# Performance work log

Hardware: AMD Instinct MI355X
Metric: run time of the kernel (lower is better)

## Reference

```python
import jax, jax.numpy as jnp
import numpy as np

B, T, D, H = 4, 1024, 512, 8
DH = D // H
MLP = 4 * D
EPS = 1e-6


def _clinear(xr, xi, Wr, Wi, br, bi):
    # Naive complex Linear = two real nn.Linear layers (each adds its own bias):
    # re = Lr(xr) - Li(xi), im = Lr(xi) + Li(xr)
    re = xr @ Wr.T - xi @ Wi.T + (br - bi)
    im = xi @ Wr.T + xr @ Wi.T + (br + bi)
    return re, im


def _cln(xr, xi):
    # NaiveComplexLayerNorm: real LayerNorm (no affine) on re and im separately
    def ln(v):
        m = jnp.mean(v, -1, keepdims=True)
        va = jnp.var(v, -1, keepdims=True)
        return (v - m) * jax.lax.rsqrt(va + EPS)
    return ln(xr), ln(xi)


def _modulate(xr, xi, shr, shi, scr, sci):
    # complex x * (1 + scale) + shift, scale/shift are [B,D] broadcast over seq
    a, b = (1.0 + scr)[:, None, :], sci[:, None, :]
    return xr * a - xi * b + shr[:, None, :], xr * b + xi * a + shi[:, None, :]


def _gate(gr, gi, xr, xi):
    a, b = gr[:, None, :], gi[:, None, :]
    return xr * a - xi * b, xr * b + xi * a


def _heads(x):  # [B,T,D] -> [B,H,T,DH]
    return x.reshape(B, T, H, DH).transpose(0, 2, 1, 3)


def reference(x_re, x_im, c_re, c_im,
              ada_Wr, ada_Wi, ada_br, ada_bi,
              q_Wr, q_Wi, q_br, q_bi,
              k_Wr, k_Wi, k_br, k_bi,
              v_Wr, v_Wi, v_br, v_bi,
              o_Wr, o_Wi, o_br, o_bi,
              f1_Wr, f1_Wi, f1_br, f1_bi,
              f2_Wr, f2_Wi, f2_br, f2_bi):
    # adaLN_modulation: complex SiLU -> complex Linear -> 6 chunks along dim 1
    sr, si = jax.nn.silu(c_re), jax.nn.silu(c_im)
    mr, mi = _clinear(sr, si, ada_Wr, ada_Wi, ada_br, ada_bi)
    sh_ar, sc_ar, g_ar, sh_mr, sc_mr, g_mr = jnp.split(mr, 6, axis=1)
    sh_ai, sc_ai, g_ai, sh_mi, sc_mi, g_mi = jnp.split(mi, 6, axis=1)

    nr, ni = _cln(x_re, x_im)
    hr, hi = _modulate(nr, ni, sh_ar, sh_ai, sc_ar, sc_ai)

    qr, qi = _clinear(hr, hi, q_Wr, q_Wi, q_br, q_bi)
    kr, ki = _clinear(hr, hi, k_Wr, k_Wi, k_br, k_bi)
    vr, vi = _clinear(hr, hi, v_Wr, v_Wi, v_br, v_bi)
    qr, qi, kr, ki, vr, vi = map(_heads, (qr, qi, kr, ki, vr, vi))

    scale = 1.0 / jnp.sqrt(jnp.float32(DH))
    # complex scores q @ k^T (no conjugation, matching plain complex matmul)
    s_re = (jnp.einsum('bhqd,bhkd->bhqk', qr, kr) - jnp.einsum('bhqd,bhkd->bhqk', qi, ki)) * scale
    s_im = (jnp.einsum('bhqd,bhkd->bhqk', qr, ki) + jnp.einsum('bhqd,bhkd->bhqk', qi, kr)) * scale
    # naive complex softmax: real softmax applied to re/im independently
    a_re = jax.nn.softmax(s_re, axis=-1)
    a_im = jax.nn.softmax(s_im, axis=-1)
    o_r = jnp.einsum('bhqk,bhkd->bhqd', a_re, vr) - jnp.einsum('bhqk,bhkd->bhqd', a_im, vi)
    o_i = jnp.einsum('bhqk,bhkd->bhqd', a_re, vi) + jnp.einsum('bhqk,bhkd->bhqd', a_im, vr)
    o_r = o_r.transpose(0, 2, 1, 3).reshape(B, T, D)
    o_i = o_i.transpose(0, 2, 1, 3).reshape(B, T, D)
    o_r, o_i = _clinear(o_r, o_i, o_Wr, o_Wi, o_br, o_bi)

    gr, gi = _gate(g_ar, g_ai, o_r, o_i)
    x_re, x_im = x_re + gr, x_im + gi

    # ---- MLP branch
    nr, ni = _cln(x_re, x_im)
    hr, hi = _modulate(nr, ni, sh_mr, sh_mi, sc_mr, sc_mi)
    hr, hi = _clinear(hr, hi, f1_Wr, f1_Wi, f1_br, f1_bi)
    hr = jax.nn.gelu(hr, approximate=True)  # ComplexGELU(tanh) per component
    hi = jax.nn.gelu(hi, approximate=True)
    hr, hi = _clinear(hr, hi, f2_Wr, f2_Wi, f2_br, f2_bi)
    gr, gi = _gate(g_mr, g_mi, hr, hi)
    return jnp.stack([x_re + gr, x_im + gi])  # [2,B,T,D] = (real, imag)


def setup_inputs() -> dict:
    key = jax.random.key(0)
    ks = iter(jax.random.split(key, 48))

    def rn(shape, s=1.0):
        return jax.random.normal(next(ks), shape, dtype=jnp.float32) * s

    inp = {'x_re': rn((B, T, D)), 'x_im': rn((B, T, D)),
           'c_re': rn((B, D)), 'c_im': rn((B, D))}

    def lin(name, din, dout):
        inp[name + '_Wr'] = rn((dout, din), 0.02)
        inp[name + '_Wi'] = rn((dout, din), 0.02)
        inp[name + '_br'] = rn((dout,), 0.02)
        inp[name + '_bi'] = rn((dout,), 0.02)

    lin('ada', D, 6 * D)
    for n in ('q', 'k', 'v', 'o'):
        lin(n, D, D)
    lin('f1', D, MLP)
    lin('f2', MLP, D)
    return inp
```

## Files before the change

kernel.cpp:

```cpp
#include <hip/hip_runtime.h>


typedef unsigned short u16;
typedef __attribute__((ext_vector_type(8))) __bf16 bf16x8;
typedef __attribute__((ext_vector_type(8))) u16    u16x8;
typedef __attribute__((ext_vector_type(4))) u16    u16x4;
typedef __attribute__((ext_vector_type(4))) float  f32x4;

#define MFMA16(a, b, c) __builtin_amdgcn_mfma_f32_16x16x32_bf16(a, b, c, 0, 0, 0)

static constexpr int Bd = 4, Td = 1024, Dd = 512, Hd = 8, DHd = 64, MLPd = 2048;

__device__ __forceinline__ u16 f2bf(float x) {
  unsigned int u = __builtin_bit_cast(unsigned int, x);
  u += 0x7fffu + ((u >> 16) & 1u);
  return (u16)(u >> 16);
}
__device__ __forceinline__ bf16x8 ldsfrag(const u16* p) {
  return __builtin_bit_cast(bf16x8, *(const u16x8*)p);
}
__device__ __forceinline__ bf16x8 negbf(bf16x8 v) {
  u16x8 u = __builtin_bit_cast(u16x8, v);
  u ^= (u16)0x8000;
  return __builtin_bit_cast(bf16x8, u);
}
__device__ __forceinline__ float gelu_tanh(float x) {
  float t = tanhf(0.7978845608028654f * (x + 0.044715f * x * x * x));
  return 0.5f * x * (1.f + t);
}

struct CJobs {
  const float* src[12];
  u16* dst[12];
  int blk_start[13];
};
__global__ __launch_bounds__(256) void convert_kernel(CJobs J) {
  const int blk = blockIdx.x;
  int jj = 0;
  while (jj < 11 && blk >= J.blk_start[jj + 1]) ++jj;
  const int idx = (blk - J.blk_start[jj]) * 256 + threadIdx.x;
  const float4 v = ((const float4*)J.src[jj])[idx];
  u16x4 o;
  o[0] = f2bf(v.x); o[1] = f2bf(v.y); o[2] = f2bf(v.z); o[3] = f2bf(v.w);
  *(u16x4*)(J.dst[jj] + (size_t)idx * 4) = o;
}

__global__ __launch_bounds__(256) void ada_kernel(
    const float* __restrict__ c_re, const float* __restrict__ c_im,
    const float* __restrict__ Wr, const float* __restrict__ Wi,
    const float* __restrict__ br, const float* __restrict__ bi,
    float* __restrict__ m_r, float* __restrict__ m_i) {
  __shared__ __align__(16) float sr[512], si[512];
  const int b = blockIdx.x / 12, nb = blockIdx.x % 12;
  const int tid = threadIdx.x;
  for (int i = tid; i < 512; i += 256) {
    const float xr = c_re[b * 512 + i], xi = c_im[b * 512 + i];
    sr[i] = xr / (1.f + __expf(-xr));
    si[i] = xi / (1.f + __expf(-xi));
  }
  __syncthreads();
  const int n = nb * 256 + tid;
  const float4* wr4 = (const float4*)(Wr + (size_t)n * 512);
  const float4* wi4 = (const float4*)(Wi + (size_t)n * 512);
  const float4* sr4 = (const float4*)sr;
  const float4* si4 = (const float4*)si;
  float ar = 0.f, ai = 0.f;
  for (int k = 0; k < 128; ++k) {
    const float4 a_ = sr4[k], b_ = si4[k], u = wr4[k], v = wi4[k];
    ar += a_.x * u.x - b_.x * v.x + a_.y * u.y - b_.y * v.y +
          a_.z * u.z - b_.z * v.z + a_.w * u.w - b_.w * v.w;
    ai += b_.x * u.x + a_.x * v.x + b_.y * u.y + a_.y * v.y +
          b_.z * u.z + a_.z * v.z + b_.w * u.w + a_.w * v.w;
  }
  m_r[(size_t)b * 3072 + n] = ar + br[n] - bi[n];
  m_i[(size_t)b * 3072 + n] = ai + br[n] + bi[n];
}

__global__ __launch_bounds__(256) void ln_mod_kernel(
    const float* __restrict__ xr, const float* __restrict__ xi,
    const float* __restrict__ mv_r, const float* __restrict__ mv_i,
    int off_sh, int off_sc,
    u16* __restrict__ hr, u16* __restrict__ hi) {
  const int row = blockIdx.x;
  const int b = row >> 10;
  const int tid = threadIdx.x;
  const float* xrp = xr + (size_t)row * 512;
  const float* xip = xi + (size_t)row * 512;
  const float r0 = xrp[tid], r1 = xrp[tid + 256];
  const float i0 = xip[tid], i1 = xip[tid + 256];
  float s0 = r0 + r1, s1 = r0 * r0 + r1 * r1;
  float s2 = i0 + i1, s3 = i0 * i0 + i1 * i1;
  #pragma unroll
  for (int o = 32; o > 0; o >>= 1) {
    s0 += __shfl_down(s0, o); s1 += __shfl_down(s1, o);
    s2 += __shfl_down(s2, o); s3 += __shfl_down(s3, o);
  }
  __shared__ float red[4][4];
  if ((tid & 63) == 0) {
    const int wv = tid >> 6;
    red[wv][0] = s0; red[wv][1] = s1; red[wv][2] = s2; red[wv][3] = s3;
  }
  __syncthreads();
  s0 = red[0][0] + red[1][0] + red[2][0] + red[3][0];
  s1 = red[0][1] + red[1][1] + red[2][1] + red[3][1];
  s2 = red[0][2] + red[1][2] + red[2][2] + red[3][2];
  s3 = red[0][3] + red[1][3] + red[2][3] + red[3][3];
  const float mr = s0 * (1.f / 512.f), mi = s2 * (1.f / 512.f);
  const float vr = s1 * (1.f / 512.f) - mr * mr;
  const float vi = s3 * (1.f / 512.f) - mi * mi;
  const float rr = rsqrtf(vr + 1e-6f), ri = rsqrtf(vi + 1e-6f);
  const float* shr = mv_r + (size_t)b * 3072 + off_sh;
  const float* shi = mv_i + (size_t)b * 3072 + off_sh;
  const float* scr = mv_r + (size_t)b * 3072 + off_sc;
  const float* sci = mv_i + (size_t)b * 3072 + off_sc;
  #pragma unroll
  for (int jj = 0; jj < 2; ++jj) {
    const int n = tid + jj * 256;
    const float nr = ((jj ? r1 : r0) - mr) * rr;
    const float ni = ((jj ? i1 : i0) - mi) * ri;
    const float a = 1.f + scr[n], bb = sci[n];
    hr[(size_t)row * 512 + n] = f2bf(nr * a - ni * bb + shr[n]);
    hi[(size_t)row * 512 + n] = f2bf(nr * bb + ni * a + shi[n]);
  }
}

template <int EPI>
__global__ __launch_bounds__(256) void cgemm_kernel(
    const u16* __restrict__ Ar, const u16* __restrict__ Ai,
    const u16* __restrict__ W0r, const u16* __restrict__ W0i,
    const float* __restrict__ b0r, const float* __restrict__ b0i,
    const u16* __restrict__ W1r, const u16* __restrict__ W1i,
    const float* __restrict__ b1r, const float* __restrict__ b1i,
    const u16* __restrict__ W2r, const u16* __restrict__ W2i,
    const float* __restrict__ b2r, const float* __restrict__ b2i,
    int K, int ntiles_per_seg, int out_ld,
    u16* __restrict__ o0r, u16* __restrict__ o0i,
    u16* __restrict__ o1r, u16* __restrict__ o1i,
    u16* __restrict__ o2r, u16* __restrict__ o2i,
    const float* __restrict__ resid_r, const float* __restrict__ resid_i,
    const float* __restrict__ gate_r, const float* __restrict__ gate_i,
    float* __restrict__ ofr, float* __restrict__ ofi) {
  const int seg = blockIdx.y / ntiles_per_seg;
  const int n0 = (blockIdx.y % ntiles_per_seg) * 64;
  const int m0 = blockIdx.x * 64;
  const u16* Wr = (seg == 0) ? W0r : (seg == 1) ? W1r : W2r;
  const u16* Wi = (seg == 0) ? W0i : (seg == 1) ? W1i : W2i;
  const float* br = (seg == 0) ? b0r : (seg == 1) ? b1r : b2r;
  const float* bi = (seg == 0) ? b0i : (seg == 1) ? b1i : b2i;
  u16* obr = (seg == 0) ? o0r : (seg == 1) ? o1r : o2r;
  u16* obi = (seg == 0) ? o0i : (seg == 1) ? o1i : o2i;

  __shared__ __align__(16) u16 sA[2][64 * 72];
  __shared__ __align__(16) u16 sB[2][64 * 72];

  const int tid = threadIdx.x;
  const int w = tid >> 6, lane = tid & 63;
  const int wm = w >> 1, wn = w & 1;
  const int q4 = lane >> 4, c = lane & 15;

  const f32x4 z = {0.f, 0.f, 0.f, 0.f};
  f32x4 accR[2][2], accI[2][2];
  for (int a = 0; a < 2; ++a)
    for (int b2 = 0; b2 < 2; ++b2) { accR[a][b2] = z; accI[a][b2] = z; }

  for (int kt = 0; kt < K; kt += 64) {
    for (int idx = tid; idx < 512; idx += 256) {
      const int row = idx >> 3, cg = idx & 7;
      const int lo = row * 72 + cg * 8;
      *(u16x8*)&sA[0][lo] = *(const u16x8*)(Ar + (size_t)(m0 + row) * K + kt + cg * 8);
      *(u16x8*)&sA[1][lo] = *(const u16x8*)(Ai + (size_t)(m0 + row) * K + kt + cg * 8);
      *(u16x8*)&sB[0][lo] = *(const u16x8*)(Wr + (size_t)(n0 + row) * K + kt + cg * 8);
      *(u16x8*)&sB[1][lo] = *(const u16x8*)(Wi + (size_t)(n0 + row) * K + kt + cg * 8);
    }
    __syncthreads();
    #pragma unroll
    for (int kc = 0; kc < 2; ++kc) {
      bf16x8 a_r[2], a_i[2], a_n[2];
      #pragma unroll
      for (int mi = 0; mi < 2; ++mi) {
        const int off = (wm * 32 + mi * 16 + c) * 72 + kc * 32 + q4 * 8;
        a_r[mi] = ldsfrag(&sA[0][off]);
        a_i[mi] = ldsfrag(&sA[1][off]);
        a_n[mi] = negbf(a_i[mi]);
      }
      #pragma unroll
      for (int ni = 0; ni < 2; ++ni) {
        const int off = (wn * 32 + ni * 16 + c) * 72 + kc * 32 + q4 * 8;
        const bf16x8 b_r = ldsfrag(&sB[0][off]);
        const bf16x8 b_i = ldsfrag(&sB[1][off]);
        #pragma unroll
        for (int mi = 0; mi < 2; ++mi) {
          accR[mi][ni] = MFMA16(a_r[mi], b_r, accR[mi][ni]);
          accR[mi][ni] = MFMA16(a_n[mi], b_i, accR[mi][ni]);
          accI[mi][ni] = MFMA16(a_i[mi], b_r, accI[mi][ni]);
          accI[mi][ni] = MFMA16(a_r[mi], b_i, accI[mi][ni]);
        }
      }
    }
    __syncthreads();
  }

  const float scale = (EPI == 0 && seg == 0) ? 0.125f : 1.f;
  #pragma unroll
  for (int mi = 0; mi < 2; ++mi)
    #pragma unroll
    for (int ni = 0; ni < 2; ++ni) {
      const int n = n0 + wn * 32 + ni * 16 + c;
      const float biasr = br[n] - bi[n];
      const float biasi = br[n] + bi[n];
      #pragma unroll
      for (int r = 0; r < 4; ++r) {
        const int m = m0 + wm * 32 + mi * 16 + q4 * 4 + r;
        const float ore = accR[mi][ni][r] + biasr;
        const float oim = accI[mi][ni][r] + biasi;
        if (EPI == 0) {
          obr[(size_t)m * out_ld + n] = f2bf(ore * scale);
          obi[(size_t)m * out_ld + n] = f2bf(oim * scale);
        } else if (EPI == 2) {
          obr[(size_t)m * out_ld + n] = f2bf(gelu_tanh(ore));
          obi[(size_t)m * out_ld + n] = f2bf(gelu_tanh(oim));
        } else {
          const int bb = m >> 10;
          const float gr = gate_r[(size_t)bb * 3072 + n];
          const float gi = gate_i[(size_t)bb * 3072 + n];
          const size_t o = (size_t)m * 512 + n;
          ofr[o] = resid_r[o] + ore * gr - oim * gi;
          ofi[o] = resid_i[o] + ore * gi + oim * gr;
        }
      }
    }
}

__global__ __launch_bounds__(256) void attn_kernel(
    const u16* __restrict__ Qr, const u16* __restrict__ Qi,
    const u16* __restrict__ Kr, const u16* __restrict__ Ki,
    const u16* __restrict__ Vr, const u16* __restrict__ Vi,
    u16* __restrict__ Or, u16* __restrict__ Oi) {
  __shared__ __align__(16) u16 sQ[2][64 * 72];
  __shared__ __align__(16) u16 sK[2][64 * 72];
  __shared__ __align__(16) u16 sV[2][64 * 72];

  const int tid = threadIdx.x;
  const int w = tid >> 6, lane = tid & 63;
  const int q4 = lane >> 4, c = lane & 15;
  const int bh = blockIdx.y, b = bh >> 3, h = bh & 7;
  const int t0 = blockIdx.x * 64;
  const size_t base = (size_t)b * Td * Dd + h * DHd;

  for (int idx = tid; idx < 512; idx += 256) {
    const int row = idx >> 3, cg = idx & 7;
    const size_t g = base + (size_t)(t0 + row) * Dd + cg * 8;
    const int lo = row * 72 + cg * 8;
    *(u16x8*)&sQ[0][lo] = *(const u16x8*)(Qr + g);
    *(u16x8*)&sQ[1][lo] = *(const u16x8*)(Qi + g);
  }
  __syncthreads();
  bf16x8 aQr[2], aQi[2], aQn[2];
  #pragma unroll
  for (int kc = 0; kc < 2; ++kc) {
    const int off = (w * 16 + c) * 72 + kc * 32 + q4 * 8;
    aQr[kc] = ldsfrag(&sQ[0][off]);
    aQi[kc] = ldsfrag(&sQ[1][off]);
    aQn[kc] = negbf(aQi[kc]);
  }

  float mst[2][4], lst[2][4];
  #pragma unroll
  for (int p = 0; p < 2; ++p)
    for (int r = 0; r < 4; ++r) { mst[p][r] = -1e30f; lst[p][r] = 0.f; }
  const f32x4 z = {0.f, 0.f, 0.f, 0.f};
  f32x4 U1[4], U2[4], U3[4], U4[4];
  for (int i = 0; i < 4; ++i) { U1[i] = z; U2[i] = z; U3[i] = z; U4[i] = z; }

  for (int kt = 0; kt < 16; ++kt) {
    for (int idx = tid; idx < 512; idx += 256) {
      const int row = idx >> 3, cg = idx & 7;
      const size_t g = base + (size_t)(kt * 64 + row) * Dd + cg * 8;
      const int lo = row * 72 + cg * 8;
      *(u16x8*)&sK[0][lo] = *(const u16x8*)(Kr + g);
      *(u16x8*)&sK[1][lo] = *(const u16x8*)(Ki + g);
      const u16x8 vvr = *(const u16x8*)(Vr + g);
      const u16x8 vvi = *(const u16x8*)(Vi + g);
      #pragma unroll
      for (int j = 0; j < 8; ++j) {
        sV[0][(cg * 8 + j) * 72 + row] = vvr[j];
        sV[1][(cg * 8 + j) * 72 + row] = vvi[j];
      }
    }
    __syncthreads();

    f32x4 S[2][4];
    #pragma unroll
    for (int nb = 0; nb < 4; ++nb) {
      f32x4 tr = z, ti = z;
      #pragma unroll
      for (int kc = 0; kc < 2; ++kc) {
        const int off = (nb * 16 + c) * 72 + kc * 32 + q4 * 8;
        const bf16x8 bKr = ldsfrag(&sK[0][off]);
        const bf16x8 bKi = ldsfrag(&sK[1][off]);
        tr = MFMA16(aQr[kc], bKr, tr);
        tr = MFMA16(aQn[kc], bKi, tr);
        ti = MFMA16(aQi[kc], bKr, ti);
        ti = MFMA16(aQr[kc], bKi, ti);
      }
      S[0][nb] = tr; S[1][nb] = ti;
    }
    __syncthreads();

    float alpha[2][4];
    #pragma unroll
    for (int p = 0; p < 2; ++p) {
      float rs[4];
      #pragma unroll
      for (int r = 0; r < 4; ++r) {
        float tm = fmaxf(fmaxf(S[p][0][r], S[p][1][r]), fmaxf(S[p][2][r], S[p][3][r]));
        #pragma unroll
        for (int o = 1; o < 16; o <<= 1) tm = fmaxf(tm, __shfl_xor(tm, o));
        const float mn = fmaxf(mst[p][r], tm);
        alpha[p][r] = __expf(mst[p][r] - mn);
        mst[p][r] = mn;
        rs[r] = 0.f;
      }
      #pragma unroll
      for (int nb = 0; nb < 4; ++nb)
        #pragma unroll
        for (int r = 0; r < 4; ++r) {
          const float pv = __expf(S[p][nb][r] - mst[p][r]);
          rs[r] += pv;
          sK[p][(w * 16 + q4 * 4 + r) * 72 + nb * 16 + c] = f2bf(pv);
        }
      #pragma unroll
      for (int r = 0; r < 4; ++r) {
        float s = rs[r];
        #pragma unroll
        for (int o = 1; o < 16; o <<= 1) s += __shfl_xor(s, o);
        lst[p][r] = lst[p][r] * alpha[p][r] + s;
      }
    }
    #pragma unroll
    for (int i = 0; i < 4; ++i)
      #pragma unroll
      for (int r = 0; r < 4; ++r) {
        U1[i][r] *= alpha[0][r]; U2[i][r] *= alpha[0][r];
        U3[i][r] *= alpha[1][r]; U4[i][r] *= alpha[1][r];
      }
    asm volatile("s_waitcnt lgkmcnt(0)" ::: "memory");
    #pragma unroll
    for (int kc = 0; kc < 2; ++kc) {
      const int poff = (w * 16 + c) * 72 + kc * 32 + q4 * 8;
      const bf16x8 aPr = ldsfrag(&sK[0][poff]);
      const bf16x8 aPi = ldsfrag(&sK[1][poff]);
      #pragma unroll
      for (int nd = 0; nd < 4; ++nd) {
        const int voff = (nd * 16 + c) * 72 + kc * 32 + q4 * 8;
        const bf16x8 bVr = ldsfrag(&sV[0][voff]);
        const bf16x8 bVi = ldsfrag(&sV[1][voff]);
        U1[nd] = MFMA16(aPr, bVr, U1[nd]);
        U2[nd] = MFMA16(aPr, bVi, U2[nd]);
        U3[nd] = MFMA16(aPi, bVr, U3[nd]);
        U4[nd] = MFMA16(aPi, bVi, U4[nd]);
      }
    }
    __syncthreads();
  }

  #pragma unroll
  for (int nd = 0; nd < 4; ++nd)
    #pragma unroll
    for (int r = 0; r < 4; ++r) {
      const int trow = t0 + w * 16 + q4 * 4 + r;
      const int d = nd * 16 + c;
      const float ilre = 1.f / lst[0][r], ilim = 1.f / lst[1][r];
      const float ore = U1[nd][r] * ilre - U4[nd][r] * ilim;
      const float oim = U2[nd][r] * ilre + U3[nd][r] * ilim;
      const size_t g = base + (size_t)trow * Dd + d;
      Or[g] = f2bf(ore);
      Oi[g] = f2bf(oim);
    }
}

extern "C" void kernel_launch(void* const* d_in, const int* in_sizes, int n_in,
                              void* d_out, int out_size, void* d_ws, size_t ws_size,
                              hipStream_t stream) {
  const float* x_re  = (const float*)d_in[0];
  const float* x_im  = (const float*)d_in[1];
  const float* c_re  = (const float*)d_in[2];
  const float* c_im  = (const float*)d_in[3];
  const float* adaWr = (const float*)d_in[4];
  const float* adaWi = (const float*)d_in[5];
  const float* adabr = (const float*)d_in[6];
  const float* adabi = (const float*)d_in[7];
  const float* qWr = (const float*)d_in[8],  *qWi = (const float*)d_in[9];
  const float* qbr = (const float*)d_in[10], *qbi = (const float*)d_in[11];
  const float* kWr = (const float*)d_in[12], *kWi = (const float*)d_in[13];
  const float* kbr = (const float*)d_in[14], *kbi = (const float*)d_in[15];
  const float* vWr = (const float*)d_in[16], *vWi = (const float*)d_in[17];
  const float* vbr = (const float*)d_in[18], *vbi = (const float*)d_in[19];
  const float* oWr = (const float*)d_in[20], *oWi = (const float*)d_in[21];
  const float* obr = (const float*)d_in[22], *obi = (const float*)d_in[23];
  const float* f1Wr = (const float*)d_in[24], *f1Wi = (const float*)d_in[25];
  const float* f1br = (const float*)d_in[26], *f1bi = (const float*)d_in[27];
  const float* f2Wr = (const float*)d_in[28], *f2Wi = (const float*)d_in[29];
  const float* f2br = (const float*)d_in[30], *f2bi = (const float*)d_in[31];

  char* wsp = (char*)d_ws;
  size_t off = 0;
  auto alloc = [&](size_t bytes) -> void* {
    void* p = wsp + off;
    off += (bytes + 255) & ~(size_t)255;
    return p;
  };
  const size_t WQ = 512 * 512, WF = 2048 * 512;
  u16* wqr = (u16*)alloc(WQ * 2); u16* wqi = (u16*)alloc(WQ * 2);
  u16* wkr = (u16*)alloc(WQ * 2); u16* wki = (u16*)alloc(WQ * 2);
  u16* wvr = (u16*)alloc(WQ * 2); u16* wvi = (u16*)alloc(WQ * 2);
  u16* wor = (u16*)alloc(WQ * 2); u16* woi = (u16*)alloc(WQ * 2);
  u16* wf1r = (u16*)alloc(WF * 2); u16* wf1i = (u16*)alloc(WF * 2);
  u16* wf2r = (u16*)alloc(WF * 2); u16* wf2i = (u16*)alloc(WF * 2);
  float* m_r = (float*)alloc(4 * 3072 * 4);
  float* m_i = (float*)alloc(4 * 3072 * 4);
  const size_t ACT = (size_t)Bd * Td * Dd;
  u16* h1r = (u16*)alloc(ACT * 2); u16* h1i = (u16*)alloc(ACT * 2);
  u16* qbr_ = (u16*)alloc(ACT * 2); u16* qbi_ = (u16*)alloc(ACT * 2);
  u16* kbr_ = (u16*)alloc(ACT * 2); u16* kbi_ = (u16*)alloc(ACT * 2);
  u16* vbr_ = (u16*)alloc(ACT * 2); u16* vbi_ = (u16*)alloc(ACT * 2);
  u16* atr = (u16*)alloc(ACT * 2); u16* ati = (u16*)alloc(ACT * 2);
  float* x2r = (float*)alloc(ACT * 4); float* x2i = (float*)alloc(ACT * 4);
  u16* h2r = h1r; u16* h2i = h1i;
  u16* f1or = qbr_;
  u16* f1oi = qbr_ + (size_t)Bd * Td * MLPd;

  CJobs J;
  const float* wsrc[12] = {qWr, qWi, kWr, kWi, vWr, vWi, oWr, oWi, f1Wr, f1Wi, f2Wr, f2Wi};
  u16* wdst[12] = {wqr, wqi, wkr, wki, wvr, wvi, wor, woi, wf1r, wf1i, wf2r, wf2i};
  int cum = 0;
  for (int j = 0; j < 12; ++j) {
    J.src[j] = wsrc[j]; J.dst[j] = wdst[j]; J.blk_start[j] = cum;
    cum += (j < 8 ? (int)WQ : (int)WF) / 1024;
  }
  J.blk_start[12] = cum;
  convert_kernel<<<cum, 256, 0, stream>>>(J);

  ada_kernel<<<48, 256, 0, stream>>>(c_re, c_im, adaWr, adaWi, adabr, adabi, m_r, m_i);

  ln_mod_kernel<<<4096, 256, 0, stream>>>(x_re, x_im, m_r, m_i, 0, 512, h1r, h1i);

  cgemm_kernel<0><<<dim3(64, 24), 256, 0, stream>>>(
      h1r, h1i, wqr, wqi, qbr, qbi, wkr, wki, kbr, kbi, wvr, wvi, vbr, vbi,
      512, 8, 512, qbr_, qbi_, kbr_, kbi_, vbr_, vbi_,
      nullptr, nullptr, nullptr, nullptr, nullptr, nullptr);

  attn_kernel<<<dim3(16, 32), 256, 0, stream>>>(qbr_, qbi_, kbr_, kbi_, vbr_, vbi_, atr, ati);

  cgemm_kernel<1><<<dim3(64, 8), 256, 0, stream>>>(
      atr, ati, wor, woi, obr, obi, wor, woi, obr, obi, wor, woi, obr, obi,
      512, 8, 512, nullptr, nullptr, nullptr, nullptr, nullptr, nullptr,
      x_re, x_im, m_r + 1024, m_i + 1024, x2r, x2i);

  ln_mod_kernel<<<4096, 256, 0, stream>>>(x2r, x2i, m_r, m_i, 1536, 2048, h2r, h2i);

  cgemm_kernel<2><<<dim3(64, 32), 256, 0, stream>>>(
      h2r, h2i, wf1r, wf1i, f1br, f1bi, wf1r, wf1i, f1br, f1bi, wf1r, wf1i, f1br, f1bi,
      512, 32, 2048, f1or, f1oi, nullptr, nullptr, nullptr, nullptr,
      nullptr, nullptr, nullptr, nullptr, nullptr, nullptr);

  float* outp = (float*)d_out;
  cgemm_kernel<3><<<dim3(64, 8), 256, 0, stream>>>(
      f1or, f1oi, wf2r, wf2i, f2br, f2bi, wf2r, wf2i, f2br, f2bi, wf2r, wf2i, f2br, f2bi,
      2048, 8, 512, nullptr, nullptr, nullptr, nullptr, nullptr, nullptr,
      x2r, x2i, m_r + 2560, m_i + 2560, outp, outp + ACT);
}
```

Measured before the change: 459.4 us.

## Pre-transpose V in QKV epilogue and register-prefetch K/V tiles in attention

The V projection epilogue now writes V transposed per (batch, head) as [d][t] using vectorized stores, so the attention kernel can fill its V tile with plain 16-byte LDS writes instead of scalar transposing scatters. The attention kernel loads Q fragments straight from global memory into registers, dropping the sQ staging buffer and one barrier. It prefetches the next K/V tile into registers while the current tile is processed, restructures the barriers, and raises wave priority around the MFMA blocks. f2bf also switches to the compiler's native bf16 conversion. The launch code must pass the transposed V layout consistently.

```diff
diff --git a/kernel.cpp b/kernel.cpp
--- a/kernel.cpp
+++ b/kernel.cpp
@@ -12,9 +12,7 @@
 static constexpr int Bd = 4, Td = 1024, Dd = 512, Hd = 8, DHd = 64, MLPd = 2048;
 
 __device__ __forceinline__ u16 f2bf(float x) {
-  unsigned int u = __builtin_bit_cast(unsigned int, x);
-  u += 0x7fffu + ((u >> 16) & 1u);
-  return (u16)(u >> 16);
+  return __builtin_bit_cast(u16, (__bf16)x);
 }
 __device__ __forceinline__ bf16x8 ldsfrag(const u16* p) {
   return __builtin_bit_cast(bf16x8, *(const u16x8*)p);
@@ -208,6 +206,19 @@
       const int n = n0 + wn * 32 + ni * 16 + c;
       const float biasr = br[n] - bi[n];
       const float biasi = br[n] + bi[n];
+      if (EPI == 0 && seg == 2) {
+        const int m = m0 + wm * 32 + mi * 16 + q4 * 4;
+        u16x4 pr, pi;
+        #pragma unroll
+        for (int r = 0; r < 4; ++r) {
+          pr[r] = f2bf(accR[mi][ni][r] + biasr);
+          pi[r] = f2bf(accI[mi][ni][r] + biasi);
+        }
+        const size_t o = ((size_t)((m >> 10) * 512 + n)) * 1024 + (m & 1023);
+        *(u16x4*)(obr + o) = pr;
+        *(u16x4*)(obi + o) = pi;
+        continue;
+      }
       #pragma unroll
       for (int r = 0; r < 4; ++r) {
         const int m = m0 + wm * 32 + mi * 16 + q4 * 4 + r;
@@ -234,9 +245,8 @@
 __global__ __launch_bounds__(256) void attn_kernel(
     const u16* __restrict__ Qr, const u16* __restrict__ Qi,
     const u16* __restrict__ Kr, const u16* __restrict__ Ki,
-    const u16* __restrict__ Vr, const u16* __restrict__ Vi,
+    const u16* __restrict__ Vtr, const u16* __restrict__ Vti,
     u16* __restrict__ Or, u16* __restrict__ Oi) {
-  __shared__ __align__(16) u16 sQ[2][64 * 72];
   __shared__ __align__(16) u16 sK[2][64 * 72];
   __shared__ __align__(16) u16 sV[2][64 * 72];
 
@@ -246,21 +256,14 @@
   const int bh = blockIdx.y, b = bh >> 3, h = bh & 7;
   const int t0 = blockIdx.x * 64;
   const size_t base = (size_t)b * Td * Dd + h * DHd;
-
-  for (int idx = tid; idx < 512; idx += 256) {
-    const int row = idx >> 3, cg = idx & 7;
-    const size_t g = base + (size_t)(t0 + row) * Dd + cg * 8;
-    const int lo = row * 72 + cg * 8;
-    *(u16x8*)&sQ[0][lo] = *(const u16x8*)(Qr + g);
-    *(u16x8*)&sQ[1][lo] = *(const u16x8*)(Qi + g);
-  }
-  __syncthreads();
+  const size_t vbase = (size_t)bh << 16;
+
   bf16x8 aQr[2], aQi[2], aQn[2];
   #pragma unroll
   for (int kc = 0; kc < 2; ++kc) {
-    const int off = (w * 16 + c) * 72 + kc * 32 + q4 * 8;
-    aQr[kc] = ldsfrag(&sQ[0][off]);
-    aQi[kc] = ldsfrag(&sQ[1][off]);
+    const size_t g = base + (size_t)(t0 + w * 16 + c) * Dd + kc * 32 + q4 * 8;
+    aQr[kc] = __builtin_bit_cast(bf16x8, *(const u16x8*)(Qr + g));
+    aQi[kc] = __builtin_bit_cast(bf16x8, *(const u16x8*)(Qi + g));
     aQn[kc] = negbf(aQi[kc]);
   }
 
@@ -272,24 +275,45 @@
   f32x4 U1[4], U2[4], U3[4], U4[4];
   for (int i = 0; i < 4; ++i) { U1[i] = z; U2[i] = z; U3[i] = z; U4[i] = z; }
 
+  const int srow = tid >> 3, scg = tid & 7;
+  u16x8 R[2][4];
+  #pragma unroll
+  for (int it = 0; it < 2; ++it) {
+    const int row = srow + it * 32;
+    const size_t gk = base + (size_t)row * Dd + scg * 8;
+    const size_t gv = vbase + (size_t)row * Td + scg * 8;
+    R[it][0] = *(const u16x8*)(Kr + gk);
+    R[it][1] = *(const u16x8*)(Ki + gk);
+    R[it][2] = *(const u16x8*)(Vtr + gv);
+    R[it][3] = *(const u16x8*)(Vti + gv);
+  }
+
   for (int kt = 0; kt < 16; ++kt) {
-    for (int idx = tid; idx < 512; idx += 256) {
-      const int row = idx >> 3, cg = idx & 7;
-      const size_t g = base + (size_t)(kt * 64 + row) * Dd + cg * 8;
-      const int lo = row * 72 + cg * 8;
-      *(u16x8*)&sK[0][lo] = *(const u16x8*)(Kr + g);
-      *(u16x8*)&sK[1][lo] = *(const u16x8*)(Ki + g);
-      const u16x8 vvr = *(const u16x8*)(Vr + g);
-      const u16x8 vvi = *(const u16x8*)(Vi + g);
-      #pragma unroll
-      for (int j = 0; j < 8; ++j) {
-        sV[0][(cg * 8 + j) * 72 + row] = vvr[j];
-        sV[1][(cg * 8 + j) * 72 + row] = vvi[j];
-      }
-    }
     __syncthreads();
+    #pragma unroll
+    for (int it = 0; it < 2; ++it) {
+      const int lo = (srow + it * 32) * 72 + scg * 8;
+      *(u16x8*)&sK[0][lo] = R[it][0];
+      *(u16x8*)&sK[1][lo] = R[it][1];
+      *(u16x8*)&sV[0][lo] = R[it][2];
+      *(u16x8*)&sV[1][lo] = R[it][3];
+    }
+    if (kt < 15) {
+      #pragma unroll
+      for (int it = 0; it < 2; ++it) {
+        const int row = srow + it * 32;
+        const size_t gk = base + (size_t)((kt + 1) * 64 + row) * Dd + scg * 8;
+        const size_t gv = vbase + (size_t)row * Td + (kt + 1) * 64 + scg * 8;
+        R[it][0] = *(const u16x8*)(Kr + gk);
+        R[it][1] = *(const u16x8*)(Ki + gk);
+        R[it][2] = *(const u16x8*)(Vtr + gv);
+        R[it][3] = *(const u16x8*)(Vti + gv);
+      }
+    }
+    __syncthreads();
 
     f32x4 S[2][4];
+    __builtin_amdgcn_s_setprio(1);
     #pragma unroll
     for (int nb = 0; nb < 4; ++nb) {
       f32x4 tr = z, ti = z;
@@ -305,6 +329,7 @@
       }
       S[0][nb] = tr; S[1][nb] = ti;
     }
+    __builtin_amdgcn_s_setprio(0);
     __syncthreads();
 
     float alpha[2][4];
@@ -345,6 +370,7 @@
         U3[i][r] *= alpha[1][r]; U4[i][r] *= alpha[1][r];
       }
     asm volatile("s_waitcnt lgkmcnt(0)" ::: "memory");
+    __builtin_amdgcn_s_setprio(1);
     #pragma unroll
     for (int kc = 0; kc < 2; ++kc) {
       const int poff = (w * 16 + c) * 72 + kc * 32 + q4 * 8;
@@ -361,7 +387,7 @@
         U4[nd] = MFMA16(aPi, bVi, U4[nd]);
       }
     }
-    __syncthreads();
+    __builtin_amdgcn_s_setprio(0);
   }
 
   #pragma unroll
```

New measurement: 460.9 us. Within noise of the previous version (+0.3%).
